# Optimization experiments

Measured on AMD Instinct MI355X. Metric: run time of the kernel, lower is better.

Reference implementation:

```python
import jax, jax.numpy as jnp
import numpy as np

B, T, F, H = 256, 512, 8, 256
DEC_STEPS = 35
BN_EPS = 1e-3


def setup_inputs() -> dict:
    key = jax.random.key(0)
    ks = jax.random.split(key, 16)
    s = 0.05
    return {
        "pulse": jax.random.normal(ks[0], (B, T, F), jnp.float32),
        "bn_gamma": jax.random.uniform(ks[1], (F,), jnp.float32, 0.5, 1.5),
        "bn_beta": jax.random.normal(ks[2], (F,), jnp.float32) * s,
        "bn_mean": jax.random.normal(ks[3], (F,), jnp.float32) * s,
        "bn_var": jax.random.uniform(ks[4], (F,), jnp.float32, 0.5, 1.5),
        "W_pe": jax.random.normal(ks[5], (F, H), jnp.float32) * s,
        "b_pe": jax.random.normal(ks[6], (H,), jnp.float32) * s,
        "embed_table": jax.random.normal(ks[7], (1, H), jnp.float32) * s,
        "W_x": jax.random.normal(ks[8], (H, 4 * H), jnp.float32) * s,
        "W_h": jax.random.normal(ks[9], (H, 4 * H), jnp.float32) * s,
        "b_lstm": jax.random.normal(ks[10], (4 * H,), jnp.float32) * s,
        "W_mlp": jax.random.normal(ks[11], (H, 2), jnp.float32) * s,
        "b_mlp": jax.random.normal(ks[12], (2,), jnp.float32) * s,
        "scale_w": jax.random.normal(ks[13], (1, 1, 2), jnp.float32),
        "scale_b": jax.random.normal(ks[14], (1, 1, 2), jnp.float32),
    }


def _lstm_cell(x, h, c, W_x, W_h, b):
    # Keras LSTMCell: gate order i, f, g(cell), o
    z = x @ W_x + h @ W_h + b  # (B, 4H)
    i, f, g, o = jnp.split(z, 4, axis=-1)
    i, f, o = jax.nn.sigmoid(i), jax.nn.sigmoid(f), jax.nn.sigmoid(o)
    g = jnp.tanh(g)
    c_new = f * c + i * g
    h_new = o * jnp.tanh(c_new)
    return h_new, c_new


def reference(pulse, bn_gamma, bn_beta, bn_mean, bn_var, W_pe, b_pe,
              embed_table, W_x, W_h, b_lstm, W_mlp, b_mlp, scale_w, scale_b):
    b_, t_, _ = pulse.shape
    # BatchNorm (inference form, axis=-1, eps=1e-3)
    x = (pulse - bn_mean) * jax.lax.rsqrt(bn_var + BN_EPS) * bn_gamma + bn_beta
    pe = x @ W_pe + b_pe  # (B, T, H)

    def enc_step(carry, xt):
        h, c = carry
        h, c = _lstm_cell(xt, h, c, W_x, W_h, b_lstm)
        return (h, c), None

    h0 = jnp.zeros((b_, H), pulse.dtype)
    (h, c), _ = jax.lax.scan(enc_step, (h0, h0), pe.transpose(1, 0, 2))

    # sequence from the same encoder state each iteration; deterministically
    inp0 = jnp.broadcast_to(embed_table[0], (b_, H))

    def dec_step(carry, _):
        h, c, inp = carry
        h, c = _lstm_cell(inp, h, c, W_x, W_h, b_lstm)
        return (h, c, h), h

    _, hs = jax.lax.scan(dec_step, (h, c, inp0), None, length=DEC_STEPS)
    hs = hs.transpose(1, 0, 2)  # (B, 35, H) == eis_embed[:, 1:, :]

    pred = hs @ W_mlp + b_mlp  # (B, 35, 2) == pred[:, 1:, :]
    eis = pred * scale_w + scale_b
    return eis
```

## Files before the change

### kernel.cpp

```cpp
#include <hip/hip_runtime.h>
#include <hip/hip_bf16.h>
#include <hip/hip_fp16.h>
#include <stdint.h>

#define BB  256
#define TT  512
#define FF  8
#define HH  256
#define H4  1024
#define DEC 35
#define NWG 16
#define MW  16

typedef __attribute__((ext_vector_type(8))) short short8v;
typedef __attribute__((ext_vector_type(4))) float f32x4;

#define OFF_PX   0
#define OFF_HHI  16384
#define OFF_HLO  32768
#define OFF_MLP  49152
#define OFF_SM   51200
#define OFF_HB32 51232
#define SMEM_TOT 67680

__device__ __forceinline__ unsigned short f2bf(float x) {
    unsigned u = __float_as_uint(x);
    u += 0x7fffu + ((u >> 16) & 1u);
    return (unsigned short)(u >> 16);
}
__device__ __forceinline__ float bf2f(unsigned s) { return __uint_as_float(s << 16); }
__device__ __forceinline__ float2 h2tof2(unsigned u) {
    __half2 h2 = *reinterpret_cast<const __half2*>(&u);
    return __half22float2(h2);
}
__device__ __forceinline__ float sigf(float x) {
    x = fminf(fmaxf(x, -30.f), 30.f);
    return 1.0f / (1.0f + __expf(-x));
}
__device__ __forceinline__ float tanh_(float x) {
    x = fminf(fmaxf(x, -15.f), 15.f);
    float e = __expf(2.0f * x);
    return (e - 1.0f) / (e + 1.0f);
}


__global__ void prep_consts(const float* __restrict__ W_pe, const float* __restrict__ b_pe,
                            const float* __restrict__ embed, const float* __restrict__ W_x,
                            const float* __restrict__ b_lstm,
                            const float* __restrict__ bn_gamma, const float* __restrict__ bn_beta,
                            const float* __restrict__ bn_mean, const float* __restrict__ bn_var,
                            __half* __restrict__ wpxh, float* __restrict__ zbias,
                            float* __restrict__ zdec0) {
    int n = blockIdx.x * 256 + threadIdx.x;
    float acc[FF];
    #pragma unroll
    for (int f = 0; f < FF; ++f) acc[f] = 0.f;
    float bsum = 0.f, dsum = 0.f;
    for (int m = 0; m < HH; ++m) {
        float wx = W_x[m * H4 + n];
        #pragma unroll
        for (int f = 0; f < FF; ++f) acc[f] = fmaf(W_pe[f * HH + m], wx, acc[f]);
        bsum = fmaf(b_pe[m], wx, bsum);
        dsum = fmaf(embed[m], wx, dsum);
    }
    float zb = b_lstm[n] + bsum;
    #pragma unroll
    for (int f = 0; f < FF; ++f) {
        float s  = bn_gamma[f] * rsqrtf(bn_var[f] + 1e-3f);
        float sh = bn_beta[f] - bn_mean[f] * s;
        wpxh[n * FF + f] = __float2half(s * acc[f]);
        zb = fmaf(sh, acc[f], zb);
    }
    zbias[n] = zb;
    zdec0[n] = b_lstm[n] + dsum;
}

__global__ void prep_wfrag(const float* __restrict__ W_x, const float* __restrict__ W_h,
                           short8v* __restrict__ whf, short8v* __restrict__ wsf) {
    int nt = blockIdx.x >> 3, kc = blockIdx.x & 7, ln = threadIdx.x;
    int n = nt * 16 + (ln & 15), q = ln >> 4;
    short8v vh, vs;
    #pragma unroll
    for (int j = 0; j < 8; ++j) {
        int k = kc * 32 + q * 8 + j;
        float wh = W_h[k * H4 + n], wx = W_x[k * H4 + n];
        vh[j] = (short)f2bf(wh);
        vs[j] = (short)f2bf(wx + wh);
    }
    whf[blockIdx.x * 64 + ln] = vh;
    wsf[blockIdx.x * 64 + ln] = vs;
}

__global__ __launch_bounds__(512) void lstm_rec5(
    const short8v* __restrict__ whf, const short8v* __restrict__ wsf,
    const uint4* __restrict__ wpx4,
    const float* __restrict__ pulse,
    const float* __restrict__ zbias, const float* __restrict__ zdec0,
    const float* __restrict__ blstm,
    const float* __restrict__ W_mlp, const float* __restrict__ b_mlp,
    const float* __restrict__ scale_w, const float* __restrict__ scale_b,
    float* __restrict__ out) {
    extern __shared__ char smem[];
    uint4*   ldsPX = (uint4*)(smem + OFF_PX);
    short8v* ldsHI = (short8v*)(smem + OFF_HHI);
    short8v* ldsLO = (short8v*)(smem + OFF_HLO);
    float*   sWmlp = (float*)(smem + OFF_MLP);
    float*   sm    = (float*)(smem + OFF_SM);
    float*   hb32  = (float*)(smem + OFF_HB32);

    const int tid = threadIdx.x, g = blockIdx.x;
    const int w = tid >> 6, ln = tid & 63;
    const int col = ln & 15, q = ln >> 4;

    int ntv[8];
    #pragma unroll
    for (int tl = 0; tl < 8; ++tl) ntv[tl] = (tl >> 1) * 16 + 2 * w + (tl & 1);

    for (int i = tid; i < 1024; i += 512) ldsPX[i] = wpx4[i];
    {
        short8v zz = {};
        for (int i = tid; i < 2 * 512; i += 512) { ldsHI[i] = zz; ldsLO[i] = zz; }
    }
    for (int i = tid; i < HH * 2; i += 512) sWmlp[i] = W_mlp[i];
    if (tid < 2) { sm[tid] = b_mlp[tid]; sm[2 + tid] = scale_w[tid]; sm[4 + tid] = scale_b[tid]; }

    float zb[8];
    #pragma unroll
    for (int tl = 0; tl < 8; ++tl) zb[tl] = zbias[ntv[tl] * 16 + col];

    float c[8];
    #pragma unroll
    for (int i = 0; i < 8; ++i) c[i] = 0.f;

    const float* pbase = pulse + (size_t)(g * MW) * TT * FF;
    int rb = 0;
    __syncthreads();

#define CHAIN8(SRC) do {                                                        \
        short8v ws0[8], ws1[8];                                                 \
        _Pragma("unroll")                                                       \
        for (int tl = 0; tl < 8; ++tl) ws0[tl] = (SRC)[(size_t)(ntv[tl] * 8 + 0) * 64 + ln]; \
        _Pragma("unroll")                                                       \
        for (int tl = 0; tl < 8; ++tl) ws1[tl] = (SRC)[(size_t)(ntv[tl] * 8 + 1) * 64 + ln]; \
        _Pragma("unroll")                                                       \
        for (int kc = 0; kc < 8; ++kc) {                                        \
            short8v ah = ldsHI[rb * 512 + kc * 64 + ln];                        \
            short8v al = ldsLO[rb * 512 + kc * 64 + ln];                        \
            if ((kc & 1) == 0) {                                                \
                _Pragma("unroll")                                               \
                for (int tl = 0; tl < 8; ++tl) {                                \
                    acc[tl] = __builtin_amdgcn_mfma_f32_16x16x32_bf16(ah, ws0[tl], acc[tl], 0, 0, 0); \
                    acc[tl] = __builtin_amdgcn_mfma_f32_16x16x32_bf16(al, ws0[tl], acc[tl], 0, 0, 0); \
                }                                                               \
                if (kc + 2 < 8) {                                               \
                    _Pragma("unroll")                                           \
                    for (int tl = 0; tl < 8; ++tl) ws0[tl] = (SRC)[(size_t)(ntv[tl] * 8 + kc + 2) * 64 + ln]; \
                }                                                               \
            } else {                                                            \
                _Pragma("unroll")                                               \
                for (int tl = 0; tl < 8; ++tl) {                                \
                    acc[tl] = __builtin_amdgcn_mfma_f32_16x16x32_bf16(ah, ws1[tl], acc[tl], 0, 0, 0); \
                    acc[tl] = __builtin_amdgcn_mfma_f32_16x16x32_bf16(al, ws1[tl], acc[tl], 0, 0, 0); \
                }                                                               \
                if (kc + 2 < 8) {                                               \
                    _Pragma("unroll")                                           \
                    for (int tl = 0; tl < 8; ++tl) ws1[tl] = (SRC)[(size_t)(ntv[tl] * 8 + kc + 2) * 64 + ln]; \
                }                                                               \
            }                                                                   \
        }                                                                       \
    } while (0)

#define GATES_WRITE(WITH_HB32) do {                                             \
        unsigned short* hHIs = (unsigned short*)(smem + OFF_HHI) + (rb ^ 1) * 4096; \
        unsigned short* hLOs = (unsigned short*)(smem + OFF_HLO) + (rb ^ 1) * 4096; \
        _Pragma("unroll")                                                       \
        for (int p = 0; p < 2; ++p)                                             \
            _Pragma("unroll")                                                   \
            for (int r = 0; r < 4; ++r) {                                       \
                float cc = sigf(acc[2 + p][r]) * c[p * 4 + r] + sigf(acc[p][r]) * tanh_(acc[4 + p][r]); \
                c[p * 4 + r] = cc;                                              \
                float hh = sigf(acc[6 + p][r]) * tanh_(cc);                     \
                unsigned short hi = f2bf(hh);                                   \
                float lo = hh - bf2f(hi);                                       \
                int ad = w * 512 + (2 * p + (col >> 3)) * 128 + (4 * q + r) * 8 + (col & 7); \
                hHIs[ad] = hi;                                                  \
                hLOs[ad] = f2bf(lo);                                            \
                if (WITH_HB32) hb32[(4 * q + r) * 257 + (32 * w + 16 * p + col)] = hh; \
            }                                                                   \
    } while (0)

    for (int t = 0; t < TT; ++t) {
        float4 xc[4][2];
        #pragma unroll
        for (int r = 0; r < 4; ++r) {
            const float* pr = pbase + (size_t)(4 * q + r) * TT * FF + (size_t)t * FF;
            xc[r][0] = ((const float4*)pr)[0];
            xc[r][1] = ((const float4*)pr)[1];
        }
        f32x4 acc[8];
        #pragma unroll
        for (int tl = 0; tl < 8; ++tl) {
            uint4 wp = ldsPX[ntv[tl] * 16 + col];
            float wv[8];
            float2 d;
            d = h2tof2(wp.x); wv[0] = d.x; wv[1] = d.y;
            d = h2tof2(wp.y); wv[2] = d.x; wv[3] = d.y;
            d = h2tof2(wp.z); wv[4] = d.x; wv[5] = d.y;
            d = h2tof2(wp.w); wv[6] = d.x; wv[7] = d.y;
            f32x4 av;
            #pragma unroll
            for (int r = 0; r < 4; ++r) {
                float s = zb[tl];
                s = fmaf(xc[r][0].x, wv[0], s); s = fmaf(xc[r][0].y, wv[1], s);
                s = fmaf(xc[r][0].z, wv[2], s); s = fmaf(xc[r][0].w, wv[3], s);
                s = fmaf(xc[r][1].x, wv[4], s); s = fmaf(xc[r][1].y, wv[5], s);
                s = fmaf(xc[r][1].z, wv[6], s); s = fmaf(xc[r][1].w, wv[7], s);
                av[r] = s;
            }
            acc[tl] = av;
        }
        CHAIN8(whf);
        GATES_WRITE(0);
        __syncthreads();
        rb ^= 1;
    }

    float zd0[8], bl[8];
    #pragma unroll
    for (int tl = 0; tl < 8; ++tl) {
        zd0[tl] = zdec0[ntv[tl] * 16 + col];
        bl[tl]  = blstm[ntv[tl] * 16 + col];
    }

    for (int s = 0; s < DEC; ++s) {
        f32x4 acc[8];
        if (s == 0) {
            #pragma unroll
            for (int tl = 0; tl < 8; ++tl) {
                f32x4 av; av[0] = zd0[tl]; av[1] = zd0[tl]; av[2] = zd0[tl]; av[3] = zd0[tl];
                acc[tl] = av;
            }
            CHAIN8(whf);
        } else {
            #pragma unroll
            for (int tl = 0; tl < 8; ++tl) {
                f32x4 av; av[0] = bl[tl]; av[1] = bl[tl]; av[2] = bl[tl]; av[3] = bl[tl];
                acc[tl] = av;
            }
            CHAIN8(wsf);
        }
        GATES_WRITE(1);
        __syncthreads();

        {
            int m = tid >> 5, j = (tid >> 4) & 1, uc = tid & 15;
            float p2 = 0.f;
            #pragma unroll
            for (int i = 0; i < 16; ++i) {
                int u = i * 16 + uc;
                p2 = fmaf(hb32[m * 257 + u], sWmlp[u * 2 + j], p2);
            }
            p2 += __shfl_down(p2, 8, 16);
            p2 += __shfl_down(p2, 4, 16);
            p2 += __shfl_down(p2, 2, 16);
            p2 += __shfl_down(p2, 1, 16);
            if (uc == 0) {
                float pr = p2 + sm[j];
                out[((size_t)(g * MW + m) * DEC + s) * 2 + j] = pr * sm[2 + j] + sm[4 + j];
            }
        }
        __syncthreads();
        rb ^= 1;
    }
#undef CHAIN8
#undef GATES_WRITE
}

__global__ void prep_weights(const float* __restrict__ Wx, const float* __restrict__ Wh,
                             __hip_bfloat16* __restrict__ wxb,
                             __hip_bfloat16* __restrict__ whb,
                             __hip_bfloat16* __restrict__ wsb) {
    int i = blockIdx.x * 256 + threadIdx.x;
    if (i < HH * H4) {
        float x = Wx[i], h = Wh[i];
        wxb[i] = __float2bfloat16(x);
        whb[i] = __float2bfloat16(h);
        wsb[i] = __float2bfloat16(x + h);
    }
}

template<bool BF16W>
__device__ __forceinline__ void matvec2(const void* __restrict__ W,
                                        const float* __restrict__ vec,
                                        int tid, float& z0, float& z1) {
    if constexpr (BF16W) {
        const uint32_t* Wp = (const uint32_t*)W;
        #pragma unroll 8
        for (int k = 0; k < HH; ++k) {
            uint32_t w = Wp[(size_t)k * (H4 / 2) + tid];
            float s = vec[k];
            union { uint32_t u; float f; } lo, hi;
            lo.u = w << 16;
            hi.u = w & 0xffff0000u;
            z0 = fmaf(s, lo.f, z0);
            z1 = fmaf(s, hi.f, z1);
        }
    } else {
        const float2* Wp = (const float2*)W;
        #pragma unroll 8
        for (int k = 0; k < HH; ++k) {
            float2 w = Wp[(size_t)k * (H4 / 2) + tid];
            float s = vec[k];
            z0 = fmaf(s, w.x, z0);
            z1 = fmaf(s, w.y, z1);
        }
    }
}

__device__ __forceinline__ float sigmoidf_(float x) { return 1.0f / (1.0f + expf(-x)); }

template<bool BF16W>
__global__ __launch_bounds__(512)
void lstm_persist(const float* __restrict__ pulse,
                  const float* __restrict__ bn_gamma, const float* __restrict__ bn_beta,
                  const float* __restrict__ bn_mean, const float* __restrict__ bn_var,
                  const float* __restrict__ W_pe, const float* __restrict__ b_pe,
                  const float* __restrict__ embed,
                  const float* __restrict__ W_x, const float* __restrict__ W_h,
                  const float* __restrict__ b_lstm,
                  const float* __restrict__ W_mlp, const float* __restrict__ b_mlp,
                  const float* __restrict__ scale_w, const float* __restrict__ scale_b,
                  const void* __restrict__ WxQ, const void* __restrict__ WhQ,
                  const void* __restrict__ WsQ,
                  float* __restrict__ out) {
    __shared__ float sWpe2[FF * HH];
    __shared__ float sbpe2[HH];
    __shared__ float sbl[H4];
    __shared__ float sWmlp[HH * 2];
    __shared__ float sbuf[HH];
    __shared__ float hbuf[HH];
    __shared__ float cbuf[HH];
    __shared__ float zbuf[H4];
    __shared__ float bnsc[FF], bnsh[FF];
    __shared__ float smisc[6];

    const int tid = threadIdx.x;
    const int bb  = blockIdx.x;

    if (tid < FF) {
        float s = bn_gamma[tid] * rsqrtf(bn_var[tid] + 1e-3f);
        bnsc[tid] = s;
        bnsh[tid] = bn_beta[tid] - bn_mean[tid] * s;
    }
    if (tid < 2) {
        smisc[tid]     = b_mlp[tid];
        smisc[2 + tid] = scale_w[tid];
        smisc[4 + tid] = scale_b[tid];
    }
    for (int i = tid; i < H4; i += 512) sbl[i] = b_lstm[i];
    for (int i = tid; i < 2 * HH; i += 512) sWmlp[i] = W_mlp[i];
    for (int i = tid; i < HH; i += 512) { hbuf[i] = 0.f; cbuf[i] = 0.f; }
    __syncthreads();
    for (int i = tid; i < FF * HH; i += 512) sWpe2[i] = W_pe[i] * bnsc[i / HH];
    for (int i = tid; i < HH; i += 512) {
        float a = b_pe[i];
        #pragma unroll
        for (int f = 0; f < FF; ++f) a = fmaf(bnsh[f], W_pe[f * HH + i], a);
        sbpe2[i] = a;
    }
    __syncthreads();
    if (tid >= HH && tid < 2 * HH) {
        int u = tid - HH;
        const float* pr = pulse + (size_t)bb * TT * FF;
        float acc = sbpe2[u];
        #pragma unroll
        for (int f = 0; f < FF; ++f) acc = fmaf(pr[f], sWpe2[f * HH + u], acc);
        sbuf[u] = acc;
    }
    __syncthreads();

    for (int t = 0; t < TT; ++t) {
        float z0 = sbl[2 * tid], z1 = sbl[2 * tid + 1];
        if constexpr (BF16W) {
            matvec2<true>(WxQ, sbuf, tid, z0, z1);
            matvec2<true>(WhQ, hbuf, tid, z0, z1);
        } else {
            matvec2<false>(W_x, sbuf, tid, z0, z1);
            matvec2<false>(W_h, hbuf, tid, z0, z1);
        }
        zbuf[2 * tid] = z0; zbuf[2 * tid + 1] = z1;
        __syncthreads();
        if (tid < HH) {
            float iv = zbuf[tid], fv = zbuf[tid + HH];
            float gv = zbuf[tid + 2 * HH], ov = zbuf[tid + 3 * HH];
            float c = sigmoidf_(fv) * cbuf[tid] + sigmoidf_(iv) * tanhf(gv);
            cbuf[tid] = c;
            hbuf[tid] = sigmoidf_(ov) * tanhf(c);
        } else if (tid < 2 * HH) {
            int u = tid - HH;
            float acc;
            if (t + 1 < TT) {
                const float* pr = pulse + ((size_t)bb * TT + (t + 1)) * FF;
                acc = sbpe2[u];
                #pragma unroll
                for (int f = 0; f < FF; ++f) acc = fmaf(pr[f], sWpe2[f * HH + u], acc);
            } else {
                acc = embed[u];
            }
            sbuf[u] = acc;
        }
        __syncthreads();
    }

    for (int s = 0; s < DEC; ++s) {
        float z0 = sbl[2 * tid], z1 = sbl[2 * tid + 1];
        if (s == 0) {
            if constexpr (BF16W) {
                matvec2<true>(WxQ, sbuf, tid, z0, z1);
                matvec2<true>(WhQ, hbuf, tid, z0, z1);
            } else {
                matvec2<false>(W_x, sbuf, tid, z0, z1);
                matvec2<false>(W_h, hbuf, tid, z0, z1);
            }
        } else {
            if constexpr (BF16W) {
                matvec2<true>(WsQ, hbuf, tid, z0, z1);
            } else {
                matvec2<false>(W_x, hbuf, tid, z0, z1);
                matvec2<false>(W_h, hbuf, tid, z0, z1);
            }
        }
        zbuf[2 * tid] = z0; zbuf[2 * tid + 1] = z1;
        __syncthreads();
        if (tid < HH) {
            float iv = zbuf[tid], fv = zbuf[tid + HH];
            float gv = zbuf[tid + 2 * HH], ov = zbuf[tid + 3 * HH];
            float c = sigmoidf_(fv) * cbuf[tid] + sigmoidf_(iv) * tanhf(gv);
            cbuf[tid] = c;
            hbuf[tid] = sigmoidf_(ov) * tanhf(c);
        }
        __syncthreads();
        if (tid < 128) {
            int j = tid >> 6, lane = tid & 63;
            float p = 0.f;
            #pragma unroll
            for (int u = lane; u < HH; u += 64) p = fmaf(hbuf[u], sWmlp[u * 2 + j], p);
            p += __shfl_down(p, 32); p += __shfl_down(p, 16); p += __shfl_down(p, 8);
            p += __shfl_down(p, 4);  p += __shfl_down(p, 2);  p += __shfl_down(p, 1);
            if (lane == 0) {
                float pr2 = p + smisc[j];
                out[((size_t)bb * DEC + s) * 2 + j] = pr2 * smisc[2 + j] + smisc[4 + j];
            }
        }
        __syncthreads();
    }
}

extern "C" void kernel_launch(void* const* d_in, const int* in_sizes, int n_in,
                              void* d_out, int out_size, void* d_ws, size_t ws_size,
                              hipStream_t stream) {
    const float* pulse    = (const float*)d_in[0];
    const float* bn_gamma = (const float*)d_in[1];
    const float* bn_beta  = (const float*)d_in[2];
    const float* bn_mean  = (const float*)d_in[3];
    const float* bn_var   = (const float*)d_in[4];
    const float* W_pe     = (const float*)d_in[5];
    const float* b_pe     = (const float*)d_in[6];
    const float* embed    = (const float*)d_in[7];
    const float* W_x      = (const float*)d_in[8];
    const float* W_h      = (const float*)d_in[9];
    const float* b_lstm   = (const float*)d_in[10];
    const float* W_mlp    = (const float*)d_in[11];
    const float* b_mlp    = (const float*)d_in[12];
    const float* scale_w  = (const float*)d_in[13];
    const float* scale_b  = (const float*)d_in[14];
    float* out = (float*)d_out;

    const size_t SZ_WF  = (size_t)64 * 8 * 64 * 16;
    const size_t SZ_PXH = (size_t)H4 * FF * 2;
    const size_t needA = 2 * SZ_WF + SZ_PXH + 2 * (size_t)H4 * 4;

    if (ws_size >= needA) {
        short8v* whf   = (short8v*)d_ws;
        short8v* wsf   = (short8v*)((char*)d_ws + SZ_WF);
        __half*  wpxh  = (__half*)((char*)d_ws + 2 * SZ_WF);
        float*   zbias = (float*)((char*)d_ws + 2 * SZ_WF + SZ_PXH);
        float*   zdec0 = zbias + H4;

        hipFuncSetAttribute((const void*)lstm_rec5,
                            hipFuncAttributeMaxDynamicSharedMemorySize, SMEM_TOT);

        prep_consts<<<4, 256, 0, stream>>>(W_pe, b_pe, embed, W_x, b_lstm,
                                           bn_gamma, bn_beta, bn_mean, bn_var,
                                           wpxh, zbias, zdec0);
        prep_wfrag<<<512, 64, 0, stream>>>(W_x, W_h, whf, wsf);
        lstm_rec5<<<NWG, 512, SMEM_TOT, stream>>>(whf, wsf, (const uint4*)wpxh, pulse,
                                                  zbias, zdec0, b_lstm,
                                                  W_mlp, b_mlp, scale_w, scale_b, out);
        return;
    }

    const size_t NW = (size_t)HH * H4;
    bool use_bf16 = ws_size >= 3 * NW * sizeof(__hip_bfloat16);
    __hip_bfloat16* wxb = (__hip_bfloat16*)d_ws;
    __hip_bfloat16* whb = wxb + NW;
    __hip_bfloat16* wsb = whb + NW;

    if (use_bf16) {
        prep_weights<<<(int)((NW + 255) / 256), 256, 0, stream>>>(W_x, W_h, wxb, whb, wsb);
        lstm_persist<true><<<BB, 512, 0, stream>>>(
            pulse, bn_gamma, bn_beta, bn_mean, bn_var, W_pe, b_pe, embed,
            W_x, W_h, b_lstm, W_mlp, b_mlp, scale_w, scale_b,
            (const void*)wxb, (const void*)whb, (const void*)wsb, out);
    } else {
        lstm_persist<false><<<BB, 512, 0, stream>>>(
            pulse, bn_gamma, bn_beta, bn_mean, bn_var, W_pe, b_pe, embed,
            W_x, W_h, b_lstm, W_mlp, b_mlp, scale_w, scale_b,
            nullptr, nullptr, nullptr, out);
    }
}
```

Baseline: 6.005 ms.

## Keep W_h fragments resident in registers and LDS instead of streaming per step

The recurrent kernel previously streamed every W_h fragment from global/L2 on each of the 512+35 steps. Now one gate tile per wave stays in registers, two tiles are cached in 128KB of LDS, and only the remaining five tiles are streamed; the input-projection weights move from LDS into registers. The double-buffered h state is replaced by a single buffer with an extra barrier per step, and the fp32 h copy for the MLP head is dropped in favour of reconstructing it from the bf16 hi/lo pair. This trades higher register and LDS pressure, plus an added sync per step, for less per-step memory traffic on the serial critical path.

After: 11.57 ms. +92.7%, slower.

```diff
diff --git a/kernel.cpp b/kernel.cpp
--- a/kernel.cpp
+++ b/kernel.cpp
@@ -15,13 +15,12 @@
 typedef __attribute__((ext_vector_type(8))) short short8v;
 typedef __attribute__((ext_vector_type(4))) float f32x4;
 
-#define OFF_PX   0
-#define OFF_HHI  16384
-#define OFF_HLO  32768
-#define OFF_MLP  49152
-#define OFF_SM   51200
-#define OFF_HB32 51232
-#define SMEM_TOT 67680
+#define OFF_LDSW 0
+#define OFF_HHI  131072
+#define OFF_HLO  139264
+#define OFF_MLP  147456
+#define OFF_SM   149504
+#define SMEM_TOT 149536
 
 __device__ __forceinline__ unsigned short f2bf(float x) {
     unsigned u = __float_as_uint(x);
@@ -91,7 +90,8 @@
     wsf[blockIdx.x * 64 + ln] = vs;
 }
 
-__global__ __launch_bounds__(512) void lstm_rec5(
+__global__ __attribute__((amdgpu_waves_per_eu(2, 2))) __launch_bounds__(512)
+void lstm_rec6(
     const short8v* __restrict__ whf, const short8v* __restrict__ wsf,
     const uint4* __restrict__ wpx4,
     const float* __restrict__ pulse,
@@ -101,12 +101,13 @@
     const float* __restrict__ scale_w, const float* __restrict__ scale_b,
     float* __restrict__ out) {
     extern __shared__ char smem[];
-    uint4*   ldsPX = (uint4*)(smem + OFF_PX);
+    short8v* ldsW  = (short8v*)(smem + OFF_LDSW);
     short8v* ldsHI = (short8v*)(smem + OFF_HHI);
     short8v* ldsLO = (short8v*)(smem + OFF_HLO);
+    unsigned short* hHIs = (unsigned short*)(smem + OFF_HHI);
+    unsigned short* hLOs = (unsigned short*)(smem + OFF_HLO);
     float*   sWmlp = (float*)(smem + OFF_MLP);
     float*   sm    = (float*)(smem + OFF_SM);
-    float*   hb32  = (float*)(smem + OFF_HB32);
 
     const int tid = threadIdx.x, g = blockIdx.x;
     const int w = tid >> 6, ln = tid & 63;
@@ -116,63 +117,101 @@
     #pragma unroll
     for (int tl = 0; tl < 8; ++tl) ntv[tl] = (tl >> 1) * 16 + 2 * w + (tl & 1);
 
-    for (int i = tid; i < 1024; i += 512) ldsPX[i] = wpx4[i];
+    #pragma unroll
+    for (int tl = 2; tl < 4; ++tl) {
+        int slot = w * 2 + (tl - 2);
+        #pragma unroll
+        for (int kc = 0; kc < 8; ++kc)
+            ldsW[(slot * 8 + kc) * 64 + ln] = whf[(size_t)(ntv[tl] * 8 + kc) * 64 + ln];
+    }
     {
         short8v zz = {};
-        for (int i = tid; i < 2 * 512; i += 512) { ldsHI[i] = zz; ldsLO[i] = zz; }
+        ldsHI[tid] = zz;
+        ldsLO[tid] = zz;
     }
     for (int i = tid; i < HH * 2; i += 512) sWmlp[i] = W_mlp[i];
     if (tid < 2) { sm[tid] = b_mlp[tid]; sm[2 + tid] = scale_w[tid]; sm[4 + tid] = scale_b[tid]; }
 
+    short8v wreg[8];
+    #pragma unroll
+    for (int kc = 0; kc < 8; ++kc)
+        wreg[kc] = whf[(size_t)(ntv[0] * 8 + kc) * 64 + ln];
+
+    uint4 wpx[8];
     float zb[8];
     #pragma unroll
-    for (int tl = 0; tl < 8; ++tl) zb[tl] = zbias[ntv[tl] * 16 + col];
+    for (int tl = 0; tl < 8; ++tl) {
+        int n = ntv[tl] * 16 + col;
+        wpx[tl] = wpx4[n];
+        zb[tl]  = zbias[n];
+    }
 
     float c[8];
     #pragma unroll
     for (int i = 0; i < 8; ++i) c[i] = 0.f;
 
     const float* pbase = pulse + (size_t)(g * MW) * TT * FF;
-    int rb = 0;
     __syncthreads();
 
-#define CHAIN8(SRC) do {                                                        \
-        short8v ws0[8], ws1[8];                                                 \
+#define MFMA2(a_idx, bsrc) do {                                                 \
+        acc[a_idx] = __builtin_amdgcn_mfma_f32_16x16x32_bf16(ah, (bsrc), acc[a_idx], 0, 0, 0); \
+        acc[a_idx] = __builtin_amdgcn_mfma_f32_16x16x32_bf16(al, (bsrc), acc[a_idx], 0, 0, 0); \
+    } while (0)
+
+#define CHAIN_RES(SRC) do {                                                     \
+        short8v ws0[5], ws1[5];                                                 \
         _Pragma("unroll")                                                       \
-        for (int tl = 0; tl < 8; ++tl) ws0[tl] = (SRC)[(size_t)(ntv[tl] * 8 + 0) * 64 + ln]; \
-        _Pragma("unroll")                                                       \
-        for (int tl = 0; tl < 8; ++tl) ws1[tl] = (SRC)[(size_t)(ntv[tl] * 8 + 1) * 64 + ln]; \
+        for (int i = 0; i < 5; ++i) {                                           \
+            const int tl_ = (i == 0) ? 1 : (i + 3);                             \
+            ws0[i] = (SRC)[(size_t)(ntv[tl_] * 8 + 0) * 64 + ln];               \
+            ws1[i] = (SRC)[(size_t)(ntv[tl_] * 8 + 1) * 64 + ln];               \
+        }                                                                       \
         _Pragma("unroll")                                                       \
         for (int kc = 0; kc < 8; ++kc) {                                        \
-            short8v ah = ldsHI[rb * 512 + kc * 64 + ln];                        \
-            short8v al = ldsLO[rb * 512 + kc * 64 + ln];                        \
-            if ((kc & 1) == 0) {                                                \
-                _Pragma("unroll")                                               \
-                for (int tl = 0; tl < 8; ++tl) {                                \
-                    acc[tl] = __builtin_amdgcn_mfma_f32_16x16x32_bf16(ah, ws0[tl], acc[tl], 0, 0, 0); \
-                    acc[tl] = __builtin_amdgcn_mfma_f32_16x16x32_bf16(al, ws0[tl], acc[tl], 0, 0, 0); \
-                }                                                               \
-                if (kc + 2 < 8) {                                               \
-                    _Pragma("unroll")                                           \
-                    for (int tl = 0; tl < 8; ++tl) ws0[tl] = (SRC)[(size_t)(ntv[tl] * 8 + kc + 2) * 64 + ln]; \
-                }                                                               \
-            } else {                                                            \
-                _Pragma("unroll")                                               \
-                for (int tl = 0; tl < 8; ++tl) {                                \
-                    acc[tl] = __builtin_amdgcn_mfma_f32_16x16x32_bf16(ah, ws1[tl], acc[tl], 0, 0, 0); \
-                    acc[tl] = __builtin_amdgcn_mfma_f32_16x16x32_bf16(al, ws1[tl], acc[tl], 0, 0, 0); \
-                }                                                               \
-                if (kc + 2 < 8) {                                               \
-                    _Pragma("unroll")                                           \
-                    for (int tl = 0; tl < 8; ++tl) ws1[tl] = (SRC)[(size_t)(ntv[tl] * 8 + kc + 2) * 64 + ln]; \
+            short8v ah = ldsHI[kc * 64 + ln];                                   \
+            short8v al = ldsLO[kc * 64 + ln];                                   \
+            MFMA2(0, wreg[kc]);                                                 \
+            { short8v b_ = ldsW[((w * 2) * 8 + kc) * 64 + ln];     MFMA2(2, b_); } \
+            { short8v b_ = ldsW[((w * 2 + 1) * 8 + kc) * 64 + ln]; MFMA2(3, b_); } \
+            _Pragma("unroll")                                                   \
+            for (int i = 0; i < 5; ++i) {                                       \
+                const int tl_ = (i == 0) ? 1 : (i + 3);                         \
+                if ((kc & 1) == 0) {                                            \
+                    MFMA2(tl_, ws0[i]);                                         \
+                    if (kc + 2 < 8) ws0[i] = (SRC)[(size_t)(ntv[tl_] * 8 + kc + 2) * 64 + ln]; \
+                } else {                                                        \
+                    MFMA2(tl_, ws1[i]);                                         \
+                    if (kc + 2 < 8) ws1[i] = (SRC)[(size_t)(ntv[tl_] * 8 + kc + 2) * 64 + ln]; \
                 }                                                               \
             }                                                                   \
         }                                                                       \
     } while (0)
 
-#define GATES_WRITE(WITH_HB32) do {                                             \
-        unsigned short* hHIs = (unsigned short*)(smem + OFF_HHI) + (rb ^ 1) * 4096; \
-        unsigned short* hLOs = (unsigned short*)(smem + OFF_HLO) + (rb ^ 1) * 4096; \
+#define CHAIN_FULL(SRC) do {                                                    \
+        short8v ws0[8], ws1[8];                                                 \
+        _Pragma("unroll")                                                       \
+        for (int i = 0; i < 8; ++i) {                                           \
+            ws0[i] = (SRC)[(size_t)(ntv[i] * 8 + 0) * 64 + ln];                 \
+            ws1[i] = (SRC)[(size_t)(ntv[i] * 8 + 1) * 64 + ln];                 \
+        }                                                                       \
+        _Pragma("unroll")                                                       \
+        for (int kc = 0; kc < 8; ++kc) {                                        \
+            short8v ah = ldsHI[kc * 64 + ln];                                   \
+            short8v al = ldsLO[kc * 64 + ln];                                   \
+            _Pragma("unroll")                                                   \
+            for (int i = 0; i < 8; ++i) {                                       \
+                if ((kc & 1) == 0) {                                            \
+                    MFMA2(i, ws0[i]);                                           \
+                    if (kc + 2 < 8) ws0[i] = (SRC)[(size_t)(ntv[i] * 8 + kc + 2) * 64 + ln]; \
+                } else {                                                        \
+                    MFMA2(i, ws1[i]);                                           \
+                    if (kc + 2 < 8) ws1[i] = (SRC)[(size_t)(ntv[i] * 8 + kc + 2) * 64 + ln]; \
+                }                                                               \
+            }                                                                   \
+        }                                                                       \
+    } while (0)
+
+#define GATES_WRITE() do {                                                      \
         _Pragma("unroll")                                                       \
         for (int p = 0; p < 2; ++p)                                             \
             _Pragma("unroll")                                                   \
@@ -185,7 +224,6 @@
                 int ad = w * 512 + (2 * p + (col >> 3)) * 128 + (4 * q + r) * 8 + (col & 7); \
                 hHIs[ad] = hi;                                                  \
                 hLOs[ad] = f2bf(lo);                                            \
-                if (WITH_HB32) hb32[(4 * q + r) * 257 + (32 * w + 16 * p + col)] = hh; \
             }                                                                   \
     } while (0)
 
@@ -200,13 +238,12 @@
         f32x4 acc[8];
         #pragma unroll
         for (int tl = 0; tl < 8; ++tl) {
-            uint4 wp = ldsPX[ntv[tl] * 16 + col];
             float wv[8];
             float2 d;
-            d = h2tof2(wp.x); wv[0] = d.x; wv[1] = d.y;
-            d = h2tof2(wp.y); wv[2] = d.x; wv[3] = d.y;
-            d = h2tof2(wp.z); wv[4] = d.x; wv[5] = d.y;
-            d = h2tof2(wp.w); wv[6] = d.x; wv[7] = d.y;
+            d = h2tof2(wpx[tl].x); wv[0] = d.x; wv[1] = d.y;
+            d = h2tof2(wpx[tl].y); wv[2] = d.x; wv[3] = d.y;
+            d = h2tof2(wpx[tl].z); wv[4] = d.x; wv[5] = d.y;
+            d = h2tof2(wpx[tl].w); wv[6] = d.x; wv[7] = d.y;
             f32x4 av;
             #pragma unroll
             for (int r = 0; r < 4; ++r) {
@@ -219,10 +256,10 @@
             }
             acc[tl] = av;
         }
-        CHAIN8(whf);
-        GATES_WRITE(0);
-        __syncthreads();
-        rb ^= 1;
+        CHAIN_RES(whf);
+        __syncthreads();
+        GATES_WRITE();
+        __syncthreads();
     }
 
     float zd0[8], bl[8];
@@ -240,16 +277,17 @@
                 f32x4 av; av[0] = zd0[tl]; av[1] = zd0[tl]; av[2] = zd0[tl]; av[3] = zd0[tl];
                 acc[tl] = av;
             }
-            CHAIN8(whf);
+            CHAIN_RES(whf);
         } else {
             #pragma unroll
             for (int tl = 0; tl < 8; ++tl) {
                 f32x4 av; av[0] = bl[tl]; av[1] = bl[tl]; av[2] = bl[tl]; av[3] = bl[tl];
                 acc[tl] = av;
             }
-            CHAIN8(wsf);
-        }
-        GATES_WRITE(1);
+            CHAIN_FULL(wsf);
+        }
+        __syncthreads();
+        GATES_WRITE();
         __syncthreads();
 
         {
@@ -258,7 +296,9 @@
             #pragma unroll
             for (int i = 0; i < 16; ++i) {
                 int u = i * 16 + uc;
-                p2 = fmaf(hb32[m * 257 + u], sWmlp[u * 2 + j], p2);
+                int ad = (u >> 5) * 512 + ((u >> 3) & 3) * 128 + m * 8 + (u & 7);
+                float hv = bf2f(hHIs[ad]) + bf2f(hLOs[ad]);
+                p2 = fmaf(hv, sWmlp[u * 2 + j], p2);
             }
             p2 += __shfl_down(p2, 8, 16);
             p2 += __shfl_down(p2, 4, 16);
@@ -269,10 +309,10 @@
                 out[((size_t)(g * MW + m) * DEC + s) * 2 + j] = pr * sm[2 + j] + sm[4 + j];
             }
         }
-        __syncthreads();
-        rb ^= 1;
-    }
-#undef CHAIN8
+    }
+#undef MFMA2
+#undef CHAIN_RES
+#undef CHAIN_FULL
 #undef GATES_WRITE
 }
 
@@ -487,14 +527,14 @@
         float*   zbias = (float*)((char*)d_ws + 2 * SZ_WF + SZ_PXH);
         float*   zdec0 = zbias + H4;
 
-        hipFuncSetAttribute((const void*)lstm_rec5,
+        hipFuncSetAttribute((const void*)lstm_rec6,
                             hipFuncAttributeMaxDynamicSharedMemorySize, SMEM_TOT);
 
         prep_consts<<<4, 256, 0, stream>>>(W_pe, b_pe, embed, W_x, b_lstm,
                                            bn_gamma, bn_beta, bn_mean, bn_var,
                                            wpxh, zbias, zdec0);
         prep_wfrag<<<512, 64, 0, stream>>>(W_x, W_h, whf, wsf);
-        lstm_rec5<<<NWG, 512, SMEM_TOT, stream>>>(whf, wsf, (const uint4*)wpxh, pulse,
+        lstm_rec6<<<NWG, 512, SMEM_TOT, stream>>>(whf, wsf, (const uint4*)wpxh, pulse,
                                                   zbias, zdec0, b_lstm,
                                                   W_mlp, b_mlp, scale_w, scale_b, out);
         return;
```
